# Kernel optimization log

Measured on AMD Instinct MI355X. Metric: run time of the kernel, lower is better.

The kernel has to match this reference:

```python
import jax
import jax.numpy as jnp
import numpy as np

B = 128            # batch size
K = 65536          # queue size
H = 768            # hidden size (BERT-base)
NUM_LABELS = 64
TOP_K = 5          # args.top_k
T = 0.07           # temperature
POS_MIN = K // NUM_LABELS          # 1024 (exact positive count per row by construction)
NEG_MIN = K - POS_MIN              # 64512 (exact negative count per row)


def setup_inputs() -> dict:
    key = jax.random.key(0)
    k1, k2 = jax.random.split(key)
    liner_q = jax.random.normal(k1, (B, H), dtype=jnp.float32)
    feature_queue = jax.random.normal(k2, (K, H), dtype=jnp.float32)
    # labels constructed so every label appears exactly K//NUM_LABELS times in the queue
    label_q = (jnp.arange(B) % NUM_LABELS).astype(jnp.int32)
    label_queue = (jnp.arange(K) % NUM_LABELS).astype(jnp.int32)
    return {
        "liner_q": liner_q,
        "feature_queue": feature_queue,
        "label_q": label_q,
        "label_queue": label_queue,
    }


def _l2norm(x):
    # matches module's l2norm: x / sqrt(sum(x^2, -1))
    norm = jnp.sqrt(jnp.sum(x * x, axis=-1, keepdims=True))
    return x / norm


def reference(liner_q, feature_queue, label_q, label_queue):
    # normalize query projections (l2norm applied to contrastive_liner_q output)
    q = _l2norm(liner_q)                                  # [B, H]
    # cos_sim = einsum('nc,nkc->nk') with queue broadcast over batch == q @ queue^T
    cos_sim = jnp.einsum("nc,kc->nk", q, feature_queue)   # [B, K]

    pos_mask = label_q[:, None] == label_queue[None, :]   # [B, K] bool
    # masked_scatter of negatives into a -inf-filled tensor
    neg_sample = jnp.where(pos_mask, -jnp.inf, cos_sim)   # [B, K]

    # torch code: cos_sim.topk(pos_min)[:, :top_k]  (topk over ALL sims, then slice)
    # pos_min (=1024) >= TOP_K, so equivalent to topk(TOP_K)
    pos_sample, _ = jax.lax.top_k(cos_sim, TOP_K)         # [B, TOP_K]
    pos_sample = pos_sample.reshape(-1, 1)                # [B*TOP_K, 1]

    # negatives: topk over -inf-masked sims, k = neg_min (exact negative count)
    neg_sorted, _ = jax.lax.top_k(neg_sample, NEG_MIN)    # [B, NEG_MIN]
    # repeat([1, neg_topk]).view([-1, neg_min]): each row repeated TOP_K times
    neg_topk = min(POS_MIN, TOP_K)                        # = TOP_K
    neg_rep = jnp.repeat(neg_sorted, neg_topk, axis=0)    # [B*TOP_K, NEG_MIN]

    logits_con = jnp.concatenate([pos_sample, neg_rep], axis=-1) / T
    return logits_con                                     # [B*TOP_K, NEG_MIN+1]
```

## Files before the change

kernel.cpp:

```cpp
#include <hip/hip_runtime.h>
#include <hip/hip_bf16.h>

#define B_SZ 128
#define K_SZ 65536
#define H_SZ 768
#define TOPK 5
#define NEG_MIN 64512
#define OUTC 64513
#define NBINS 65536
#define INV_T (1.0f/0.07f)

typedef __attribute__((ext_vector_type(8))) short short8;
typedef __attribute__((ext_vector_type(4))) float f32x4;

__device__ __forceinline__ unsigned short f32_bf16(float v) {
    unsigned u = __float_as_uint(v);
    unsigned r = ((u >> 16) & 1u) + 0x7FFFu;
    return (unsigned short)((u + r) >> 16);
}
__device__ __forceinline__ unsigned f32_key(float v) {
    unsigned u = __float_as_uint(v);
    unsigned r = ((u >> 16) & 1u) + 0x7FFFu;
    unsigned b = (u + r) >> 16;
    return (b & 0x8000u) ? (0xFFFFu & ~b) : (b | 0x8000u);
}
__device__ __forceinline__ float key_val(unsigned key) {
    unsigned b = (key & 0x8000u) ? (key ^ 0x8000u) : (0xFFFFu & ~key);
    return __uint_as_float(b << 16);
}

__global__ __launch_bounds__(256) void norm_kernel(const float* __restrict__ q,
                                                   unsigned short* __restrict__ qn) {
    __shared__ float red[256];
    const int b = blockIdx.x, t = threadIdx.x;
    float s = 0.f;
    for (int h = t; h < H_SZ; h += 256) { float v = q[b*H_SZ + h]; s += v*v; }
    red[t] = s; __syncthreads();
    for (int off = 128; off > 0; off >>= 1) {
        if (t < off) red[t] += red[t + off];
        __syncthreads();
    }
    const float inv = 1.0f / sqrtf(red[0]);
    for (int h = t; h < H_SZ; h += 256) qn[b*H_SZ + h] = f32_bf16(q[b*H_SZ + h] * inv);
}

__global__ __launch_bounds__(256) void gemm_key_kernel(
    const unsigned short* __restrict__ qn, const float* __restrict__ fq,
    unsigned* __restrict__ hist)
{
    __shared__ unsigned short Fs[128][40];
    __shared__ unsigned short Qs[128][40];
    const int tid  = threadIdx.x;
    const int lane = tid & 63;
    const int w    = tid >> 6;
    const int k_base = blockIdx.x * 128;

    f32x4 acc[2][8];
#pragma unroll
    for (int mg = 0; mg < 2; ++mg)
#pragma unroll
        for (int bg = 0; bg < 8; ++bg) acc[mg][bg] = (f32x4){0.f, 0.f, 0.f, 0.f};

    for (int kc = 0; kc < H_SZ/32; ++kc) {
        const int c0 = kc * 32;
        __syncthreads();
#pragma unroll
        for (int it = 0; it < 4; ++it) {
            const int task = it*256 + tid;
            const int r = task >> 3, q = task & 7;
            const float4 v = *(const float4*)(fq + (size_t)(k_base + r)*H_SZ + c0 + q*4);
            ushort4 b4;
            b4.x = f32_bf16(v.x); b4.y = f32_bf16(v.y);
            b4.z = f32_bf16(v.z); b4.w = f32_bf16(v.w);
            *(ushort4*)(&Fs[r][q*4]) = b4;
        }
#pragma unroll
        for (int it = 0; it < 2; ++it) {
            const int task = it*256 + tid;
            const int r = task >> 2, h = task & 3;
            const uint4 v = *(const uint4*)(qn + (size_t)r*H_SZ + c0 + h*8);
            *(uint4*)(&Qs[r][h*8]) = v;
        }
        __syncthreads();
        const int ko = (lane >> 4) * 8;
        short8 a[2], bq[8];
        a[0] = *(const short8*)(&Fs[w*32      + (lane & 15)][ko]);
        a[1] = *(const short8*)(&Fs[w*32 + 16 + (lane & 15)][ko]);
#pragma unroll
        for (int bg = 0; bg < 8; ++bg)
            bq[bg] = *(const short8*)(&Qs[bg*16 + (lane & 15)][ko]);
#pragma unroll
        for (int mg = 0; mg < 2; ++mg)
#pragma unroll
            for (int bg = 0; bg < 8; ++bg)
                acc[mg][bg] = __builtin_amdgcn_mfma_f32_16x16x32_bf16(
                    a[mg], bq[bg], acc[mg][bg], 0, 0, 0);
    }

    const int col  = lane & 15;
    const int rgrp = (lane >> 4) * 4;
#pragma unroll
    for (int mg = 0; mg < 2; ++mg)
#pragma unroll
        for (int bg = 0; bg < 8; ++bg) {
            ushort4 kk;
            kk.x = (unsigned short)f32_key(acc[mg][bg][0]);
            kk.y = (unsigned short)f32_key(acc[mg][bg][1]);
            kk.z = (unsigned short)f32_key(acc[mg][bg][2]);
            kk.w = (unsigned short)f32_key(acc[mg][bg][3]);
            unsigned short* dst = (unsigned short*)(hist + (size_t)(bg*16 + col)*NBINS)
                                  + (k_base + w*32 + mg*16 + rgrp);
            *(ushort4*)dst = kk;
        }
}

__global__ __launch_bounds__(256) void hist_kernel(
    const int* __restrict__ lq, const int* __restrict__ lk,
    unsigned* __restrict__ hist)
{
    __shared__ unsigned packed[NBINS/2];
    __shared__ unsigned short plist[1152];
    __shared__ unsigned pcount;
    const int row = blockIdx.x, t = threadIdx.x;
#pragma unroll
    for (int i = 0; i < 128; ++i) packed[i*256 + t] = 0;
    if (t == 0) pcount = 0;
    const int myl = lq[row];
    unsigned* hrow = hist + (size_t)row*NBINS;
    const uint4* kp = (const uint4*)hrow;
    __syncthreads();

    for (int it = 0; it < 32; ++it) {
        const int idx = it*256 + t;
        const uint4 kv = kp[idx];
        const int4 l0 = ((const int4*)lk)[idx*2];
        const int4 l1 = ((const int4*)lk)[idx*2 + 1];
        unsigned ks[8] = { kv.x & 0xFFFFu, kv.x >> 16, kv.y & 0xFFFFu, kv.y >> 16,
                           kv.z & 0xFFFFu, kv.z >> 16, kv.w & 0xFFFFu, kv.w >> 16 };
        int ls[8] = { l0.x, l0.y, l0.z, l0.w, l1.x, l1.y, l1.z, l1.w };
#pragma unroll
        for (int j = 0; j < 8; ++j) {
            atomicAdd(&packed[ks[j] >> 1], (ks[j] & 1u) ? 0x10000u : 1u);
            if (ls[j] == myl) {
                unsigned p = atomicAdd(&pcount, 1u);
                if (p < 1152) plist[p] = (unsigned short)ks[j];
            }
        }
    }
    __syncthreads();
    for (int i = 0; i < 32; ++i) {
        const int idx = i*256 + t;
        const uint4 pw = ((const uint4*)packed)[idx];
        uint4 o0, o1;
        o0.x = pw.x & 0xFFFFu; o0.y = pw.x >> 16; o0.z = pw.y & 0xFFFFu; o0.w = pw.y >> 16;
        o1.x = pw.z & 0xFFFFu; o1.y = pw.z >> 16; o1.z = pw.w & 0xFFFFu; o1.w = pw.w >> 16;
        ((uint4*)hrow)[idx*2]     = o0;
        ((uint4*)hrow)[idx*2 + 1] = o1;
    }
    __syncthreads();
    const unsigned np = pcount < 1152u ? pcount : 1152u;
    for (unsigned p = t; p < np; p += 256)
        atomicAdd(&hrow[plist[p]], 0xFFFFu);
}

__device__ __forceinline__ void wave_scan2(int lane, unsigned& sn, unsigned& sa) {
#pragma unroll
    for (int off = 1; off < 64; off <<= 1) {
        unsigned un = __shfl_up(sn, off, 64);
        unsigned ua = __shfl_up(sa, off, 64);
        if (lane >= off) { sn += un; sa += ua; }
    }
}

__global__ __launch_bounds__(256) void scan_kernel(
    const unsigned* __restrict__ hist, unsigned* __restrict__ offs)
{
    __shared__ unsigned cn[256], ca[256];
    __shared__ unsigned wn[4], wa[4];
    const int row = blockIdx.x, t = threadIdx.x;
    const int wv = t >> 6, lane = t & 63;
    const uint4* hp = (const uint4*)(hist + (size_t)row*NBINS);
    for (int i = 0; i < 64; ++i) {
        const uint4 v = hp[i*256 + t];
        unsigned n = (v.x & 0xFFFFu) + (v.y & 0xFFFFu) + (v.z & 0xFFFFu) + (v.w & 0xFFFFu);
        unsigned a = (v.x >> 16)     + (v.y >> 16)     + (v.z >> 16)     + (v.w >> 16);
#pragma unroll
        for (int off = 1; off < 64; off <<= 1) {
            n += __shfl_xor(n, off, 64);
            a += __shfl_xor(a, off, 64);
        }
        if (lane == 0) { cn[i*4 + wv] = n; ca[i*4 + wv] = a; }
    }
    __syncthreads();
    const unsigned vn = cn[255 - t];
    const unsigned va = ca[255 - t] + vn;
    unsigned sn = vn, sa = va;
    wave_scan2(lane, sn, sa);
    if (lane == 63) { wn[wv] = sn; wa[wv] = sa; }
    __syncthreads();
    unsigned pn = 0, pa = 0;
    for (int i = 0; i < wv; ++i) { pn += wn[i]; pa += wa[i]; }
    offs[((size_t)row*256 + t)*2 + 0] = pn + sn - vn;
    offs[((size_t)row*256 + t)*2 + 1] = pa + sa - va;
}

__global__ __launch_bounds__(256) void emit_kernel(
    const unsigned* __restrict__ hist, const unsigned* __restrict__ offs,
    float* __restrict__ out)
{
    __shared__ unsigned wn[4], wa[4];
    __shared__ unsigned cum[257];
    __shared__ float vals[256];
    const int c = blockIdx.x, row = blockIdx.y, t = threadIdx.x;
    const int wv = t >> 6, lane = t & 63;
    const unsigned key = 65535u - (unsigned)(c*256 + t);
    const unsigned w   = hist[(size_t)row*NBINS + key];
    const unsigned neg = w & 0xFFFFu;
    const unsigned all = neg + (w >> 16);
    unsigned sn = neg, sa = all;
    wave_scan2(lane, sn, sa);
    if (lane == 63) { wn[wv] = sn; wa[wv] = sa; }
    __syncthreads();
    unsigned pn = 0, pa = 0;
    for (int i = 0; i < wv; ++i) { pn += wn[i]; pa += wa[i]; }
    const unsigned eneg = pn + sn - neg;
    const unsigned eall = pa + sa - all;
    const float val = key_val(key) * INV_T;
    vals[t] = val;
    cum[t + 1] = pn + sn;
    if (t == 0) cum[0] = 0;

    const unsigned ba = offs[((size_t)row*256 + c)*2 + 1] + eall;
    if (ba < TOPK && all > 0) {
        const unsigned end = (ba + all < TOPK) ? (ba + all) : TOPK;
        for (unsigned r = ba; r < end; ++r)
            out[((size_t)row*TOPK + r)*OUTC] = val;
    }
    __syncthreads();

    const unsigned S    = cum[256];
    const unsigned base = offs[((size_t)row*256 + c)*2 + 0];
    float* orow = out + (size_t)row*TOPK*OUTC + 1 + base;
    for (unsigned e = t; e < S; e += 256) {
        unsigned lo = 0, hi = 255;
#pragma unroll
        for (int i = 0; i < 8; ++i) {
            const unsigned mid = (lo + hi) >> 1;
            if (cum[mid + 1] > e) hi = mid; else lo = mid + 1;
        }
        const float v = vals[lo];
        orow[e]          = v;
        orow[OUTC   + e] = v;
        orow[2*OUTC + e] = v;
        orow[3*OUTC + e] = v;
        orow[4*OUTC + e] = v;
    }
}

extern "C" void kernel_launch(void* const* d_in, const int* in_sizes, int n_in,
                              void* d_out, int out_size, void* d_ws, size_t ws_size,
                              hipStream_t stream)
{
    (void)in_sizes; (void)n_in; (void)out_size; (void)ws_size;
    const float* liner_q = (const float*)d_in[0];
    const float* fq      = (const float*)d_in[1];
    const int*   lq      = (const int*)d_in[2];
    const int*   lk      = (const int*)d_in[3];
    float* out = (float*)d_out;

    char* ws = (char*)d_ws;
    unsigned short* qn   = (unsigned short*)ws;
    unsigned*       offs = (unsigned*)(ws + 196608);
    unsigned*       hist = (unsigned*)(ws + 458752);

    norm_kernel<<<B_SZ, 256, 0, stream>>>(liner_q, qn);
    gemm_key_kernel<<<K_SZ/128, 256, 0, stream>>>(qn, fq, hist);
    hist_kernel<<<B_SZ, 256, 0, stream>>>(lq, lk, hist);
    scan_kernel<<<B_SZ, 256, 0, stream>>>(hist, offs);
    emit_kernel<<<dim3(256, B_SZ), 256, 0, stream>>>(hist, offs, out);
}
```

Measured before the change: 548.7 us.

## Coarsen emit kernel to 8 segments per row and move top-k emit to scan

The emit kernel now processes 8192 bins per block (8 blocks per row instead of 256). It builds a padded shared-memory prefix sum over the segment's negative counts and binary-searches 13 levels to map each output element to its bin. Writing the top-5 positive values moves into the scan kernel, where the thread whose chunk contains the first ranks walks the histogram serially. The goal is to cut the block count and the redundant per-block scan and launch overhead. The trade-off is much lower parallelism (1024 blocks), a larger shared-memory footprint and a longer search per output element.

```diff
diff --git a/kernel.cpp b/kernel.cpp
--- a/kernel.cpp
+++ b/kernel.cpp
@@ -9,6 +9,8 @@
 #define OUTC 64513
 #define NBINS 65536
 #define INV_T (1.0f/0.07f)
+#define SEGS 8
+#define SEG_BINS 8192
 
 typedef __attribute__((ext_vector_type(8))) short short8;
 typedef __attribute__((ext_vector_type(4))) float f32x4;
@@ -28,6 +30,7 @@
     unsigned b = (key & 0x8000u) ? (key ^ 0x8000u) : (0xFFFFu & ~key);
     return __uint_as_float(b << 16);
 }
+__device__ __forceinline__ int fpad(int d) { return d + (d >> 5); }
 
 __global__ __launch_bounds__(256) void norm_kernel(const float* __restrict__ q,
                                                    unsigned short* __restrict__ qn) {
@@ -173,7 +176,8 @@
 }
 
 __global__ __launch_bounds__(256) void scan_kernel(
-    const unsigned* __restrict__ hist, unsigned* __restrict__ offs)
+    const unsigned* __restrict__ hist, unsigned* __restrict__ offs,
+    float* __restrict__ out)
 {
     __shared__ unsigned cn[256], ca[256];
     __shared__ unsigned wn[4], wa[4];
@@ -200,55 +204,88 @@
     __syncthreads();
     unsigned pn = 0, pa = 0;
     for (int i = 0; i < wv; ++i) { pn += wn[i]; pa += wa[i]; }
-    offs[((size_t)row*256 + t)*2 + 0] = pn + sn - vn;
-    offs[((size_t)row*256 + t)*2 + 1] = pa + sa - va;
+    const unsigned eneg = pn + sn - vn;
+    const unsigned eall = pa + sa - va;
+    offs[((size_t)row*256 + t)*2 + 0] = eneg;
+    offs[((size_t)row*256 + t)*2 + 1] = eall;
+
+    if (eall < TOPK) {
+        const unsigned* hrow = hist + (size_t)row*NBINS;
+        unsigned r = eall;
+        for (int j = 0; j < 256 && r < TOPK; ++j) {
+            const unsigned key = 65535u - (unsigned)(t*256 + j);
+            const unsigned w = hrow[key];
+            const unsigned cnt = (w & 0xFFFFu) + (w >> 16);
+            if (cnt) {
+                const float val = key_val(key) * INV_T;
+                unsigned end = r + cnt; if (end > TOPK) end = TOPK;
+                for (unsigned rr = r; rr < end; ++rr)
+                    out[((size_t)row*TOPK + rr)*OUTC] = val;
+                r += cnt;
+            }
+        }
+    }
 }
 
 __global__ __launch_bounds__(256) void emit_kernel(
     const unsigned* __restrict__ hist, const unsigned* __restrict__ offs,
     float* __restrict__ out)
 {
-    __shared__ unsigned wn[4], wa[4];
-    __shared__ unsigned cum[257];
-    __shared__ float vals[256];
-    const int c = blockIdx.x, row = blockIdx.y, t = threadIdx.x;
-    const int wv = t >> 6, lane = t & 63;
-    const unsigned key = 65535u - (unsigned)(c*256 + t);
-    const unsigned w   = hist[(size_t)row*NBINS + key];
-    const unsigned neg = w & 0xFFFFu;
-    const unsigned all = neg + (w >> 16);
-    unsigned sn = neg, sa = all;
-    wave_scan2(lane, sn, sa);
-    if (lane == 63) { wn[wv] = sn; wa[wv] = sa; }
-    __syncthreads();
-    unsigned pn = 0, pa = 0;
-    for (int i = 0; i < wv; ++i) { pn += wn[i]; pa += wa[i]; }
-    const unsigned eneg = pn + sn - neg;
-    const unsigned eall = pa + sa - all;
-    const float val = key_val(key) * INV_T;
-    vals[t] = val;
-    cum[t + 1] = pn + sn;
-    if (t == 0) cum[0] = 0;
-
-    const unsigned ba = offs[((size_t)row*256 + c)*2 + 1] + eall;
-    if (ba < TOPK && all > 0) {
-        const unsigned end = (ba + all < TOPK) ? (ba + all) : TOPK;
-        for (unsigned r = ba; r < end; ++r)
-            out[((size_t)row*TOPK + r)*OUTC] = val;
-    }
-    __syncthreads();
-
-    const unsigned S    = cum[256];
-    const unsigned base = offs[((size_t)row*256 + c)*2 + 0];
+    __shared__ unsigned A[8449];
+    __shared__ unsigned tsum[256];
+    __shared__ unsigned wsum[4];
+    const int s = blockIdx.x, row = blockIdx.y, t = threadIdx.x;
+    const unsigned* hrow = hist + (size_t)row*NBINS;
+
+    for (int j = 0; j < 32; ++j) {
+        const int d = j*256 + t;
+        const unsigned key = 65535u - (unsigned)(s*SEG_BINS + d);
+        A[fpad(d + 1)] = hrow[key] & 0xFFFFu;
+    }
+    __syncthreads();
+    unsigned run = 0;
+#pragma unroll
+    for (int i = 0; i < 32; ++i) {
+        const int d = t*32 + 1 + i;
+        run += A[fpad(d)];
+        A[fpad(d)] = run;
+    }
+    tsum[t] = run;
+    __syncthreads();
+    {
+        const int wv = t >> 6, lane = t & 63;
+        unsigned v = tsum[t], sv = v;
+#pragma unroll
+        for (int off = 1; off < 64; off <<= 1) {
+            unsigned u = __shfl_up(sv, off, 64);
+            if (lane >= off) sv += u;
+        }
+        if (lane == 63) wsum[wv] = sv;
+        __syncthreads();
+        unsigned p = 0;
+        for (int i = 0; i < wv; ++i) p += wsum[i];
+        const unsigned excl = p + sv - v;
+#pragma unroll
+        for (int i = 0; i < 32; ++i) {
+            const int d = t*32 + 1 + i;
+            A[fpad(d)] += excl;
+        }
+        if (t == 0) A[fpad(0)] = 0;
+    }
+    __syncthreads();
+
+    const unsigned S    = A[fpad(8192)];
+    const unsigned base = offs[((size_t)row*256 + s*32)*2 + 0];
     float* orow = out + (size_t)row*TOPK*OUTC + 1 + base;
     for (unsigned e = t; e < S; e += 256) {
-        unsigned lo = 0, hi = 255;
-#pragma unroll
-        for (int i = 0; i < 8; ++i) {
-            const unsigned mid = (lo + hi) >> 1;
-            if (cum[mid + 1] > e) hi = mid; else lo = mid + 1;
-        }
-        const float v = vals[lo];
+        int lo = 0, hi = 8191;
+#pragma unroll
+        for (int i = 0; i < 13; ++i) {
+            const int mid = (lo + hi) >> 1;
+            if (A[fpad(mid + 1)] > e) hi = mid; else lo = mid + 1;
+        }
+        const unsigned key = 65535u - (unsigned)(s*SEG_BINS + lo);
+        const float v = key_val(key) * INV_T;
         orow[e]          = v;
         orow[OUTC   + e] = v;
         orow[2*OUTC + e] = v;
@@ -276,6 +313,6 @@
     norm_kernel<<<B_SZ, 256, 0, stream>>>(liner_q, qn);
     gemm_key_kernel<<<K_SZ/128, 256, 0, stream>>>(qn, fq, hist);
     hist_kernel<<<B_SZ, 256, 0, stream>>>(lq, lk, hist);
-    scan_kernel<<<B_SZ, 256, 0, stream>>>(hist, offs);
-    emit_kernel<<<dim3(256, B_SZ), 256, 0, stream>>>(hist, offs, out);
-}
+    scan_kernel<<<B_SZ, 256, 0, stream>>>(hist, offs, out);
+    emit_kernel<<<dim3(SEGS, B_SZ), 256, 0, stream>>>(hist, offs, out);
+}
```

Measured after the change: 558.7 us. No clear change (+1.8%).
